# Performance work log

Hardware: AMD Instinct MI355X
Metric: run time of the kernel (lower is better)

The kernel has to match this reference:

```python
import jax, jax.numpy as jnp
import numpy as np

N_NODES = 50000
N_EDGES = 800000
IN_CH = 128
HID = 64
MLP_HID = 128
EPS = 1e-5


def setup_inputs() -> dict:
    key = jax.random.key(0)
    ks = iter(jax.random.split(key, 32))
    d = {}
    d['x'] = jax.random.normal(next(ks), (N_NODES, IN_CH), dtype=jnp.float32)
    d['edge_index'] = jax.random.randint(next(ks), (2, N_EDGES), 0, N_NODES, dtype=jnp.int64)

    def lin(k, out_c, in_c, scale=None):
        s = scale if scale is not None else 1.0 / np.sqrt(in_c)
        return jax.random.uniform(k, (out_c, in_c), jnp.float32, -s, s)

    # layer 0: in->hid, with residual linear
    d['Wl0'] = lin(next(ks), HID, IN_CH); d['bl0'] = jnp.zeros((HID,), jnp.float32)
    d['Wr0'] = lin(next(ks), HID, IN_CH)
    d['g0'] = jnp.ones((HID,), jnp.float32); d['be0'] = jnp.zeros((HID,), jnp.float32)
    d['rW0'] = lin(next(ks), HID, IN_CH); d['rb0'] = jnp.zeros((HID,), jnp.float32)
    # layers 1,2: hid->hid, identity residual
    for i in (1, 2):
        d[f'Wl{i}'] = lin(next(ks), HID, HID); d[f'bl{i}'] = jnp.zeros((HID,), jnp.float32)
        d[f'Wr{i}'] = lin(next(ks), HID, HID)
        d[f'g{i}'] = jnp.ones((HID,), jnp.float32); d[f'be{i}'] = jnp.zeros((HID,), jnp.float32)
    # edge MLP: 2*HID -> MLP_HID -> MLP_HID -> 1
    d['W1'] = lin(next(ks), MLP_HID, 2 * HID); d['b1'] = jnp.zeros((MLP_HID,), jnp.float32)
    d['W2'] = lin(next(ks), MLP_HID, MLP_HID); d['b2'] = jnp.zeros((MLP_HID,), jnp.float32)
    d['W3'] = lin(next(ks), 1, MLP_HID); d['b3'] = jnp.zeros((1,), jnp.float32)
    return d


def _res_sage_layer(x, src, tgt, Wl, bl, Wr, g, be, rW=None, rb=None):
    # SAGEConv (mean aggr): out = lin_l(mean_{j in N(i)} x_j) + lin_r(x_i)
    msg = x[src]                                              # [E, C] gather
    agg = jax.ops.segment_sum(msg, tgt, num_segments=N_NODES)
    cnt = jax.ops.segment_sum(jnp.ones((msg.shape[0],), x.dtype), tgt, num_segments=N_NODES)
    mean = agg / jnp.maximum(cnt, 1.0)[:, None]
    out = mean @ Wl.T + bl + x @ Wr.T
    # BatchNorm (training-mode batch statistics, biased var)
    mu = out.mean(axis=0)
    var = out.var(axis=0)
    out = (out - mu) * jax.lax.rsqrt(var + EPS) * g + be
    out = jax.nn.relu(out)
    res = x @ rW.T + rb if rW is not None else x
    return out + res


def reference(x, edge_index, Wl0, bl0, Wr0, g0, be0, rW0, rb0,
              Wl1, bl1, Wr1, g1, be1, Wl2, bl2, Wr2, g2, be2,
              W1, b1, W2, b2, W3, b3):
    src, tgt = edge_index[0], edge_index[1]
    h = _res_sage_layer(x, src, tgt, Wl0, bl0, Wr0, g0, be0, rW0, rb0)
    h = _res_sage_layer(h, src, tgt, Wl1, bl1, Wr1, g1, be1)
    h = _res_sage_layer(h, src, tgt, Wl2, bl2, Wr2, g2, be2)
    edge_repr = jnp.concatenate([h[src], h[tgt]], axis=1)     # [E, 2*HID]
    z = jax.nn.relu(edge_repr @ W1.T + b1)                    # dropout: eval mode (identity)
    z = jax.nn.relu(z @ W2.T + b2)
    return z @ W3.T + b3                                      # [E, 1]
```

## Files before the change

kernel.cpp:

```cpp
#include <hip/hip_runtime.h>
#include <hip/hip_bf16.h>

#define NN 50000
#define NE 800000
#define HID 64
#define EPSV 1e-5f
#define NBLK 196

typedef __attribute__((ext_vector_type(8))) short bf16x8;
typedef __attribute__((ext_vector_type(4))) float f32x4;
typedef __attribute__((ext_vector_type(4))) int int4v;

__device__ __forceinline__ ushort f2b(float f) {
    union { __hip_bfloat16 b; ushort u; } c;
    c.b = __float2bfloat16(f);
    return c.u;
}
__device__ __forceinline__ float b2f(ushort u) {
    return __uint_as_float(((unsigned int)u) << 16);
}

__global__ void prep_w_kernel(const float* __restrict__ W1, const float* __restrict__ W2,
                              ushort* __restrict__ W1b, ushort* __restrict__ W2b) {
    int i = blockIdx.x * 256 + threadIdx.x;
    if (i < 16384) W1b[i] = f2b(W1[i]);
    else           W2b[i - 16384] = f2b(W2[i - 16384]);
}

__global__ void prep_nodew_kernel(
    const float* __restrict__ Wl0, const float* __restrict__ Wr0, const float* __restrict__ rW0,
    const float* __restrict__ Wl1, const float* __restrict__ Wr1,
    const float* __restrict__ Wl2, const float* __restrict__ Wr2,
    ushort* __restrict__ wnb)
{
    int i = blockIdx.x * 256 + threadIdx.x;
    if      (i < 8192)  wnb[i] = f2b(Wl0[i]);
    else if (i < 16384) wnb[i] = f2b(Wr0[i - 8192]);
    else if (i < 24576) wnb[i] = f2b(rW0[i - 16384]);
    else if (i < 28672) wnb[i] = f2b(Wl1[i - 24576]);
    else if (i < 32768) wnb[i] = f2b(Wr1[i - 28672]);
    else if (i < 36864) wnb[i] = f2b(Wl2[i - 32768]);
    else if (i < 40960) wnb[i] = f2b(Wr2[i - 36864]);
}

__global__ void xcvt_kernel(const float* __restrict__ x, ushort* __restrict__ xq) {
    int i = blockIdx.x * 256 + threadIdx.x;
    float4 a = *(const float4*)&x[i * 8];
    float4 b = *(const float4*)&x[i * 8 + 4];
    union { ushort u[8]; int4v v; } pk;
    pk.u[0] = f2b(a.x); pk.u[1] = f2b(a.y); pk.u[2] = f2b(a.z); pk.u[3] = f2b(a.w);
    pk.u[4] = f2b(b.x); pk.u[5] = f2b(b.y); pk.u[6] = f2b(b.z); pk.u[7] = f2b(b.w);
    *(int4v*)&xq[i * 8] = pk.v;
}

__global__ void count_kernel(const int* __restrict__ tgt, int* __restrict__ icnt) {
    int e = blockIdx.x * 256 + threadIdx.x;
    if (e < NE) atomicAdd(&icnt[tgt[e]], 1);
}

__global__ void scan1_kernel(const int* __restrict__ icnt, int* __restrict__ off,
                             int* __restrict__ bsum) {
    __shared__ int s[256];
    const int t = threadIdx.x;
    const int i = blockIdx.x * 256 + t;
    int v = (i < NN) ? icnt[i] : 0;
    s[t] = v;
    __syncthreads();
    for (int d = 1; d < 256; d <<= 1) {
        int x = (t >= d) ? s[t - d] : 0;
        __syncthreads();
        s[t] += x;
        __syncthreads();
    }
    if (i < NN) off[i] = s[t];
    if (t == 255) bsum[blockIdx.x] = s[255];
}

__global__ void scan2_kernel(const int* __restrict__ bsum, int* __restrict__ bpre) {
    __shared__ int s[256];
    const int t = threadIdx.x;
    int v = (t < NBLK) ? bsum[t] : 0;
    s[t] = v;
    __syncthreads();
    for (int d = 1; d < 256; d <<= 1) {
        int x = (t >= d) ? s[t - d] : 0;
        __syncthreads();
        s[t] += x;
        __syncthreads();
    }
    if (t < NBLK) bpre[t] = s[t] - v;
}

__global__ void scan3_kernel(const int* __restrict__ icnt, const int* __restrict__ bpre,
                             int* __restrict__ off, int* __restrict__ woff) {
    const int i = blockIdx.x * 256 + threadIdx.x;
    if (i < NN) {
        int e = off[i] - icnt[i] + bpre[blockIdx.x];
        off[i] = e;
        woff[i] = e;
        if (i == NN - 1) off[NN] = NE;
    }
}

__global__ void fill_kernel(const int* __restrict__ src, const int* __restrict__ tgt,
                            int* __restrict__ woff, int* __restrict__ ebuf) {
    int e = blockIdx.x * 256 + threadIdx.x;
    if (e < NE) {
        int p = atomicAdd(&woff[tgt[e]], 1);
        ebuf[p] = src[e];
    }
}

template<int K>
__global__ __launch_bounds__(256) void proj_mfma_kernel(
    const ushort* __restrict__ Ab,
    const ushort* __restrict__ w0, const ushort* __restrict__ w1,
    const ushort* __restrict__ w2,
    const float* __restrict__ bias1, const float* __restrict__ bias2,
    ushort* __restrict__ xb, float* __restrict__ pre, float* __restrict__ res)
{
    __shared__ float sC[128][65];
    const int tid = threadIdx.x;
    const int wv = tid >> 6, lane = tid & 63;
    const int l15 = lane & 15, l4 = lane >> 4;
    const int seg = blockIdx.y;
    const ushort* W = (seg == 0) ? w0 : ((seg == 1) ? w1 : w2);
    const int n0 = blockIdx.x * 128;
    constexpr int KS = K / 32;

    bf16x8 wf[4][KS];
    #pragma unroll
    for (int n = 0; n < 4; n++)
        #pragma unroll
        for (int ks = 0; ks < KS; ks++)
            wf[n][ks] = *(const bf16x8*)&W[(n * 16 + l15) * K + ks * 32 + l4 * 8];

    f32x4 acc[2][4];
    #pragma unroll
    for (int m = 0; m < 2; m++)
        #pragma unroll
        for (int n = 0; n < 4; n++)
            acc[m][n] = (f32x4){0.f, 0.f, 0.f, 0.f};

    #pragma unroll
    for (int m = 0; m < 2; m++) {
        int row = n0 + wv * 32 + m * 16 + l15;
        if (row > NN - 1) row = NN - 1;
        #pragma unroll
        for (int ks = 0; ks < KS; ks++) {
            bf16x8 a = *(const bf16x8*)&Ab[(long)row * K + ks * 32 + l4 * 8];
            #pragma unroll
            for (int n = 0; n < 4; n++)
                acc[m][n] = __builtin_amdgcn_mfma_f32_16x16x32_bf16(a, wf[n][ks], acc[m][n], 0, 0, 0);
        }
    }
    #pragma unroll
    for (int m = 0; m < 2; m++)
        #pragma unroll
        for (int n = 0; n < 4; n++)
            #pragma unroll
            for (int r = 0; r < 4; r++)
                sC[wv * 32 + m * 16 + l4 * 4 + r][n * 16 + l15] = acc[m][n][r];
    __syncthreads();

    const int r = tid >> 1, ch = (tid & 1) * 32;
    const int node = n0 + r;
    if (node < NN) {
        if (seg == 0) {
            #pragma unroll
            for (int g = 0; g < 4; g++) {
                union { ushort u[8]; int4v v; } pk;
                #pragma unroll
                for (int j = 0; j < 8; j++)
                    pk.u[j] = f2b(sC[r][ch + g * 8 + j]);
                *(int4v*)&xb[(long)node * 64 + ch + g * 8] = pk.v;
            }
        } else {
            float* O = (seg == 1) ? pre : res;
            const float* bp = (seg == 1) ? bias1 : bias2;
            #pragma unroll
            for (int g = 0; g < 8; g++) {
                int c = ch + g * 4;
                float4 v = make_float4(sC[r][c + 0] + bp[c + 0], sC[r][c + 1] + bp[c + 1],
                                       sC[r][c + 2] + bp[c + 2], sC[r][c + 3] + bp[c + 3]);
                *(float4*)&O[(long)node * 64 + c] = v;
            }
        }
    }
}

__global__ __launch_bounds__(256) void gather_bn_kernel(
    const int* __restrict__ off, const int* __restrict__ ebuf,
    const ushort* __restrict__ xb,
    float* __restrict__ vbase,
    float* __restrict__ bnsum, float* __restrict__ bnsq)
{
    __shared__ float r1[4][64], r2[4][64];
    const int lane = threadIdx.x & 63;
    const int wid = __builtin_amdgcn_readfirstlane(threadIdx.x >> 6);
    float s = 0.f, q = 0.f;
    for (int n = blockIdx.x * 4 + wid; n < NN; n += gridDim.x * 4) {
        const int a = off[n], b = off[n + 1];
        float a0 = 0.f, a1 = 0.f, a2 = 0.f, a3 = 0.f;
        int p = a;
        for (; p + 4 <= b; p += 4) {
            int s0 = ebuf[p], s1 = ebuf[p + 1], s2 = ebuf[p + 2], s3 = ebuf[p + 3];
            a0 += b2f(xb[(long)s0 * 64 + lane]);
            a1 += b2f(xb[(long)s1 * 64 + lane]);
            a2 += b2f(xb[(long)s2 * 64 + lane]);
            a3 += b2f(xb[(long)s3 * 64 + lane]);
        }
        for (; p < b; ++p) a0 += b2f(xb[(long)ebuf[p] * 64 + lane]);
        float acc = (a0 + a1) + (a2 + a3);
        float v = acc / fmaxf((float)(b - a), 1.f) + vbase[(long)n * 64 + lane];
        vbase[(long)n * 64 + lane] = v;
        s += v; q += v * v;
    }
    r1[wid][lane] = s; r2[wid][lane] = q;
    __syncthreads();
    if (threadIdx.x < 64) {
        s = r1[0][lane] + r1[1][lane] + r1[2][lane] + r1[3][lane];
        q = r2[0][lane] + r2[1][lane] + r2[2][lane] + r2[3][lane];
        atomicAdd(&bnsum[lane], s);
        atomicAdd(&bnsq[lane], q);
    }
}

__global__ void apply_bn_kernel(const float* __restrict__ vbase,
                                const float* __restrict__ resbase,
                                const float* __restrict__ bnsum, const float* __restrict__ bnsq,
                                const float* __restrict__ g, const float* __restrict__ be,
                                float* __restrict__ h, ushort* __restrict__ hb)
{
    const float inv_n = 1.0f / (float)NN;
    const int stride = gridDim.x * 256;
    for (int i = blockIdx.x * 256 + threadIdx.x; i < NN * 16; i += stride) {
        int n = i >> 4;
        int c0 = (i & 15) * 4;
        float sc[4], sh[4];
        #pragma unroll
        for (int j = 0; j < 4; j++) {
            int c = c0 + j;
            float mu = bnsum[c] * inv_n;
            float var = bnsq[c] * inv_n - mu * mu;
            float rstd = rsqrtf(var + EPSV);
            sc[j] = g[c] * rstd;
            sh[j] = be[c] - mu * sc[j];
        }
        float4 v = *(const float4*)&vbase[(long)n * 64 + c0];
        float4 r = *(const float4*)&resbase[(long)n * 64 + c0];
        float4 o;
        o.x = fmaxf(fmaf(v.x, sc[0], sh[0]), 0.f) + r.x;
        o.y = fmaxf(fmaf(v.y, sc[1], sh[1]), 0.f) + r.y;
        o.z = fmaxf(fmaf(v.z, sc[2], sh[2]), 0.f) + r.z;
        o.w = fmaxf(fmaf(v.w, sc[3], sh[3]), 0.f) + r.w;
        *(float4*)&h[(long)n * 64 + c0] = o;
        union { ushort u[4]; uint2 v2; } p;
        p.u[0] = f2b(o.x); p.u[1] = f2b(o.y); p.u[2] = f2b(o.z); p.u[3] = f2b(o.w);
        *(uint2*)&hb[(long)n * 64 + c0] = p.v2;
    }
}

#define NTILE 6250
#define EMG 256
#define Z1B(row, usc) ((((row) * 272) + ((usc) * 2)) ^ ((((row) >> 1) & 7) << 4))

#define GATHER(tt)                                                        \
    do {                                                                  \
        int e0g = (t0 + (tt)) * 128;                                      \
        _Pragma("unroll")                                                 \
        for (int m = 0; m < 2; m++) {                                     \
            int e = e0g + we * 32 + m * 16 + l15;                         \
            const ushort* hs = hb + (long)src[e] * 64;                    \
            const ushort* ht = hb + (long)tgt[e] * 64;                    \
            ga[m][0] = *(const bf16x8*)&hs[l4 * 8];                       \
            ga[m][1] = *(const bf16x8*)&hs[32 + l4 * 8];                  \
            ga[m][2] = *(const bf16x8*)&ht[l4 * 8];                       \
            ga[m][3] = *(const bf16x8*)&ht[32 + l4 * 8];                  \
        }                                                                 \
    } while (0)

__global__ __launch_bounds__(512, 2) void edge_mlp_lds_kernel(
    const ushort* __restrict__ hb,
    const int* __restrict__ src, const int* __restrict__ tgt,
    const ushort* __restrict__ W1b, const ushort* __restrict__ W2b,
    const float* __restrict__ b1, const float* __restrict__ b2,
    const float* __restrict__ W3, const float* __restrict__ b3,
    float* __restrict__ out)
{
    __shared__ ushort wlds[32768];
    __shared__ ushort z1[128 * 136];
    __shared__ float red[2][2][128];

    const int tid = threadIdx.x;
    const int wid = tid >> 6, lane = tid & 63;
    const int l15 = lane & 15, l4 = lane >> 4;
    const int we = wid >> 1, wo = wid & 1;
    const int ocb = wo * 64;

    for (int c = tid; c < 4096; c += 512) {
        int layer = c >> 11, oc = (c >> 4) & 127, kc = c & 15;
        const ushort* Wsrc = layer ? W2b : W1b;
        int4v v = *(const int4v*)&Wsrc[oc * 128 + kc * 8];
        int byte = layer * 32768 + oc * 256 + ((kc * 16) ^ ((oc & 7) << 4));
        *(int4v*)((char*)wlds + byte) = v;
    }

    float b1v[4], b2v[4], w3v[4];
    #pragma unroll
    for (int n = 0; n < 4; n++) {
        int oc = ocb + n * 16 + l15;
        b1v[n] = b1[oc]; b2v[n] = b2[oc]; w3v[n] = W3[oc];
    }
    const float b3v = b3[0];

    const int bid = blockIdx.x;
    const int q = NTILE / EMG, r = NTILE % EMG;
    const int t0 = bid * q + (bid < r ? bid : r);
    const int nt = q + (bid < r ? 1 : 0);

    bf16x8 ga[2][4];
    GATHER(0);
    __syncthreads();

    for (int t = 0; t < nt; t++) {
        f32x4 acc[2][4];
        #pragma unroll
        for (int m = 0; m < 2; m++)
            #pragma unroll
            for (int n = 0; n < 4; n++)
                acc[m][n] = (f32x4){b1v[n], b1v[n], b1v[n], b1v[n]};
        #pragma unroll
        for (int ks = 0; ks < 4; ks++) {
            bf16x8 wf[4];
            #pragma unroll
            for (int n = 0; n < 4; n++) {
                int oc = ocb + n * 16 + l15;
                int byte = oc * 256 + (((ks * 4 + l4) * 16) ^ ((oc & 7) << 4));
                wf[n] = *(const bf16x8*)((const char*)wlds + byte);
            }
            #pragma unroll
            for (int m = 0; m < 2; m++)
                #pragma unroll
                for (int n = 0; n < 4; n++)
                    acc[m][n] = __builtin_amdgcn_mfma_f32_16x16x32_bf16(ga[m][ks], wf[n], acc[m][n], 0, 0, 0);
        }
        #pragma unroll
        for (int m = 0; m < 2; m++)
            #pragma unroll
            for (int n = 0; n < 4; n++) {
                int col = ocb + n * 16 + l15;
                #pragma unroll
                for (int rr = 0; rr < 4; rr++) {
                    int row = we * 32 + m * 16 + l4 * 4 + rr;
                    *(ushort*)((char*)z1 + Z1B(row, col)) = f2b(fmaxf(acc[m][n][rr], 0.f));
                }
            }
        __syncthreads();

        if (t + 1 < nt) GATHER(t + 1);

        f32x4 acc2[2][4];
        #pragma unroll
        for (int m = 0; m < 2; m++)
            #pragma unroll
            for (int n = 0; n < 4; n++)
                acc2[m][n] = (f32x4){b2v[n], b2v[n], b2v[n], b2v[n]};
        #pragma unroll
        for (int ks = 0; ks < 4; ks++) {
            bf16x8 wf[4];
            #pragma unroll
            for (int n = 0; n < 4; n++) {
                int oc = ocb + n * 16 + l15;
                int byte = 32768 + oc * 256 + (((ks * 4 + l4) * 16) ^ ((oc & 7) << 4));
                wf[n] = *(const bf16x8*)((const char*)wlds + byte);
            }
            bf16x8 a2[2];
            #pragma unroll
            for (int m = 0; m < 2; m++) {
                int erow = we * 32 + m * 16 + l15;
                a2[m] = *(const bf16x8*)((const char*)z1 + Z1B(erow, ks * 32 + l4 * 8));
            }
            #pragma unroll
            for (int m = 0; m < 2; m++)
                #pragma unroll
                for (int n = 0; n < 4; n++)
                    acc2[m][n] = __builtin_amdgcn_mfma_f32_16x16x32_bf16(a2[m], wf[n], acc2[m][n], 0, 0, 0);
        }

        #pragma unroll
        for (int m = 0; m < 2; m++)
            #pragma unroll
            for (int rr = 0; rr < 4; rr++) {
                float s = 0.f;
                #pragma unroll
                for (int n = 0; n < 4; n++)
                    s = fmaf(fmaxf(acc2[m][n][rr], 0.f), w3v[n], s);
                s += __shfl_xor(s, 1);
                s += __shfl_xor(s, 2);
                s += __shfl_xor(s, 4);
                s += __shfl_xor(s, 8);
                if (l15 == 0)
                    red[t & 1][wo][we * 32 + m * 16 + l4 * 4 + rr] = s;
            }
        __syncthreads();
        if (tid < 128)
            out[(t0 + t) * 128 + tid] = red[t & 1][0][tid] + red[t & 1][1][tid] + b3v;
    }
}

extern "C" void kernel_launch(void* const* d_in, const int* in_sizes, int n_in,
                              void* d_out, int out_size, void* d_ws, size_t ws_size,
                              hipStream_t stream)
{
    const float* x   = (const float*)d_in[0];
    const int*   ei  = (const int*)d_in[1];
    const int* src = ei;
    const int* tgt = ei + NE;
    const float* Wl0 = (const float*)d_in[2];
    const float* bl0 = (const float*)d_in[3];
    const float* Wr0 = (const float*)d_in[4];
    const float* g0  = (const float*)d_in[5];
    const float* be0 = (const float*)d_in[6];
    const float* rW0 = (const float*)d_in[7];
    const float* rb0 = (const float*)d_in[8];
    const float* Wl1 = (const float*)d_in[9];
    const float* bl1 = (const float*)d_in[10];
    const float* Wr1 = (const float*)d_in[11];
    const float* g1  = (const float*)d_in[12];
    const float* be1 = (const float*)d_in[13];
    const float* Wl2 = (const float*)d_in[14];
    const float* bl2 = (const float*)d_in[15];
    const float* Wr2 = (const float*)d_in[16];
    const float* g2  = (const float*)d_in[17];
    const float* be2 = (const float*)d_in[18];
    const float* W1  = (const float*)d_in[19];
    const float* b1  = (const float*)d_in[20];
    const float* W2  = (const float*)d_in[21];
    const float* b2  = (const float*)d_in[22];
    const float* W3  = (const float*)d_in[23];
    const float* b3  = (const float*)d_in[24];
    float* out = (float*)d_out;

    float* ws = (float*)d_ws;
    float*  pre  = ws;
    float*  res  = ws + 3200000;
    float*  hbuf = ws + 6400000;
    float*  bn   = ws + 9600000;
    float*  bnsum = bn, *bnsq = bn + 64;
    ushort* xb   = (ushort*)(ws + 9600256);
    ushort* hb   = (ushort*)(ws + 11200256);
    ushort* W1b  = (ushort*)(ws + 12800256);
    ushort* W2b  = W1b + 16384;
    int*    icnt = (int*)(ws + 12816640);
    int*    off  = icnt + 50000;
    int*    woff = off + 50001;
    int*    ebuf = woff + 50000;
    int*    bsum = ebuf + 800000;
    int*    bpre = bsum + 256;
    ushort* wnb  = (ushort*)(ws + 13767153);
    ushort* Wl0b = wnb;
    ushort* Wr0b = wnb + 8192;
    ushort* rW0b = wnb + 16384;
    ushort* Wl1b = wnb + 24576;
    ushort* Wr1b = wnb + 28672;
    ushort* Wl2b = wnb + 32768;
    ushort* Wr2b = wnb + 36864;
    ushort* xb16 = (ushort*)hbuf;

    prep_w_kernel<<<128, 256, 0, stream>>>(W1, W2, W1b, W2b);
    prep_nodew_kernel<<<160, 256, 0, stream>>>(Wl0, Wr0, rW0, Wl1, Wr1, Wl2, Wr2, wnb);
    xcvt_kernel<<<3125, 256, 0, stream>>>(x, xb16);
    hipMemsetAsync(icnt, 0, NN * sizeof(int), stream);
    count_kernel<<<NE / 256, 256, 0, stream>>>(tgt, icnt);
    scan1_kernel<<<NBLK, 256, 0, stream>>>(icnt, off, bsum);
    scan2_kernel<<<1, 256, 0, stream>>>(bsum, bpre);
    scan3_kernel<<<NBLK, 256, 0, stream>>>(icnt, bpre, off, woff);
    fill_kernel<<<NE / 256, 256, 0, stream>>>(src, tgt, woff, ebuf);

    dim3 g0g(391, 3), g12g(391, 2);

    hipMemsetAsync(bnsum, 0, 128 * sizeof(float), stream);
    proj_mfma_kernel<128><<<g0g, 256, 0, stream>>>(xb16, Wl0b, Wr0b, rW0b,
                                                   bl0, rb0, xb, pre, res);
    gather_bn_kernel<<<1024, 256, 0, stream>>>(off, ebuf, xb, pre, bnsum, bnsq);
    apply_bn_kernel<<<1024, 256, 0, stream>>>(pre, res, bnsum, bnsq, g0, be0, hbuf, hb);

    hipMemsetAsync(bnsum, 0, 128 * sizeof(float), stream);
    proj_mfma_kernel<64><<<g12g, 256, 0, stream>>>(hb, Wl1b, Wr1b, nullptr,
                                                   bl1, nullptr, xb, pre, res);
    gather_bn_kernel<<<1024, 256, 0, stream>>>(off, ebuf, xb, pre, bnsum, bnsq);
    apply_bn_kernel<<<1024, 256, 0, stream>>>(pre, hbuf, bnsum, bnsq, g1, be1, hbuf, hb);

    hipMemsetAsync(bnsum, 0, 128 * sizeof(float), stream);
    proj_mfma_kernel<64><<<g12g, 256, 0, stream>>>(hb, Wl2b, Wr2b, nullptr,
                                                   bl2, nullptr, xb, pre, res);
    gather_bn_kernel<<<1024, 256, 0, stream>>>(off, ebuf, xb, pre, bnsum, bnsq);
    apply_bn_kernel<<<1024, 256, 0, stream>>>(pre, hbuf, bnsum, bnsq, g2, be2, hbuf, hb);

    edge_mlp_lds_kernel<<<EMG, 512, 0, stream>>>(hb, src, tgt, W1b, W2b, b1, b2, W3, b3, out);
}
```

Measured before the change: 482.1 us.

## Make each wave own a full 32-edge strip in edge MLP, removing block barriers

Restructures the edge MLP kernel so each wave processes independent 32-edge strips across all 128 output channels, with a private LDS scratch for the layer-1 activations. This removes the per-tile __syncthreads barriers and the cross-wave reduction buffer, and each wave writes its outputs directly as float4. The cost is double the accumulator registers per wave (acc arrays of 2x8) and dropping the min-2-blocks launch bound, which may lower occupancy or cause spills. The z1 swizzle is replaced by a padded stride, so LDS bank conflicts may change.

```diff
diff --git a/kernel.cpp b/kernel.cpp
--- a/kernel.cpp
+++ b/kernel.cpp
@@ -261,16 +261,16 @@
     }
 }
 
-#define NTILE 6250
+#define NSTRIP 25000
 #define EMG 256
-#define Z1B(row, usc) ((((row) * 272) + ((usc) * 2)) ^ ((((row) >> 1) & 7) << 4))
-
-#define GATHER(tt)                                                        \
+#define ZSTR 136
+
+#define GATHER(ss)                                                        \
     do {                                                                  \
-        int e0g = (t0 + (tt)) * 128;                                      \
+        int e0g = (ss) * 32;                                              \
         _Pragma("unroll")                                                 \
         for (int m = 0; m < 2; m++) {                                     \
-            int e = e0g + we * 32 + m * 16 + l15;                         \
+            int e = e0g + m * 16 + l15;                                   \
             const ushort* hs = hb + (long)src[e] * 64;                    \
             const ushort* ht = hb + (long)tgt[e] * 64;                    \
             ga[m][0] = *(const bf16x8*)&hs[l4 * 8];                       \
@@ -280,7 +280,7 @@
         }                                                                 \
     } while (0)
 
-__global__ __launch_bounds__(512, 2) void edge_mlp_lds_kernel(
+__global__ __launch_bounds__(512) void edge_mlp_wave_kernel(
     const ushort* __restrict__ hb,
     const int* __restrict__ src, const int* __restrict__ tgt,
     const ushort* __restrict__ W1b, const ushort* __restrict__ W2b,
@@ -289,14 +289,11 @@
     float* __restrict__ out)
 {
     __shared__ ushort wlds[32768];
-    __shared__ ushort z1[128 * 136];
-    __shared__ float red[2][2][128];
+    __shared__ ushort z1[8][32 * ZSTR];
 
     const int tid = threadIdx.x;
     const int wid = tid >> 6, lane = tid & 63;
     const int l15 = lane & 15, l4 = lane >> 4;
-    const int we = wid >> 1, wo = wid & 1;
-    const int ocb = wo * 64;
 
     for (int c = tid; c < 4096; c += 512) {
         int layer = c >> 11, oc = (c >> 4) & 127, kc = c & 15;
@@ -306,106 +303,105 @@
         *(int4v*)((char*)wlds + byte) = v;
     }
 
-    float b1v[4], b2v[4], w3v[4];
+    float b1v[8], b2v[8], w3v[8];
     #pragma unroll
-    for (int n = 0; n < 4; n++) {
-        int oc = ocb + n * 16 + l15;
+    for (int n = 0; n < 8; n++) {
+        int oc = n * 16 + l15;
         b1v[n] = b1[oc]; b2v[n] = b2[oc]; w3v[n] = W3[oc];
     }
     const float b3v = b3[0];
 
     const int bid = blockIdx.x;
-    const int q = NTILE / EMG, r = NTILE % EMG;
+    const int q = NSTRIP / EMG, r = NSTRIP % EMG;
     const int t0 = bid * q + (bid < r ? bid : r);
     const int nt = q + (bid < r ? 1 : 0);
+    ushort* zw = z1[wid];
 
     bf16x8 ga[2][4];
-    GATHER(0);
+    if (wid < nt) GATHER(t0 + wid);
     __syncthreads();
 
-    for (int t = 0; t < nt; t++) {
-        f32x4 acc[2][4];
+    for (int j = wid; j < nt; j += 8) {
+        const int e0 = (t0 + j) * 32;
+
+        f32x4 acc[2][8];
         #pragma unroll
         for (int m = 0; m < 2; m++)
             #pragma unroll
-            for (int n = 0; n < 4; n++)
+            for (int n = 0; n < 8; n++)
                 acc[m][n] = (f32x4){b1v[n], b1v[n], b1v[n], b1v[n]};
         #pragma unroll
         for (int ks = 0; ks < 4; ks++) {
-            bf16x8 wf[4];
-            #pragma unroll
-            for (int n = 0; n < 4; n++) {
-                int oc = ocb + n * 16 + l15;
+            bf16x8 wf[8];
+            #pragma unroll
+            for (int n = 0; n < 8; n++) {
+                int oc = n * 16 + l15;
                 int byte = oc * 256 + (((ks * 4 + l4) * 16) ^ ((oc & 7) << 4));
                 wf[n] = *(const bf16x8*)((const char*)wlds + byte);
             }
             #pragma unroll
             for (int m = 0; m < 2; m++)
                 #pragma unroll
-                for (int n = 0; n < 4; n++)
+                for (int n = 0; n < 8; n++)
                     acc[m][n] = __builtin_amdgcn_mfma_f32_16x16x32_bf16(ga[m][ks], wf[n], acc[m][n], 0, 0, 0);
         }
         #pragma unroll
         for (int m = 0; m < 2; m++)
             #pragma unroll
-            for (int n = 0; n < 4; n++) {
-                int col = ocb + n * 16 + l15;
+            for (int n = 0; n < 8; n++) {
+                int col = n * 16 + l15;
                 #pragma unroll
-                for (int rr = 0; rr < 4; rr++) {
-                    int row = we * 32 + m * 16 + l4 * 4 + rr;
-                    *(ushort*)((char*)z1 + Z1B(row, col)) = f2b(fmaxf(acc[m][n][rr], 0.f));
-                }
-            }
-        __syncthreads();
-
-        if (t + 1 < nt) GATHER(t + 1);
-
-        f32x4 acc2[2][4];
+                for (int rr = 0; rr < 4; rr++)
+                    zw[(m * 16 + l4 * 4 + rr) * ZSTR + col] = f2b(fmaxf(acc[m][n][rr], 0.f));
+            }
+
+        if (j + 8 < nt) GATHER(t0 + j + 8);
+
+        f32x4 acc2[2][8];
         #pragma unroll
         for (int m = 0; m < 2; m++)
             #pragma unroll
-            for (int n = 0; n < 4; n++)
+            for (int n = 0; n < 8; n++)
                 acc2[m][n] = (f32x4){b2v[n], b2v[n], b2v[n], b2v[n]};
         #pragma unroll
         for (int ks = 0; ks < 4; ks++) {
-            bf16x8 wf[4];
-            #pragma unroll
-            for (int n = 0; n < 4; n++) {
-                int oc = ocb + n * 16 + l15;
+            bf16x8 wf[8];
+            #pragma unroll
+            for (int n = 0; n < 8; n++) {
+                int oc = n * 16 + l15;
                 int byte = 32768 + oc * 256 + (((ks * 4 + l4) * 16) ^ ((oc & 7) << 4));
                 wf[n] = *(const bf16x8*)((const char*)wlds + byte);
             }
             bf16x8 a2[2];
             #pragma unroll
-            for (int m = 0; m < 2; m++) {
-                int erow = we * 32 + m * 16 + l15;
-                a2[m] = *(const bf16x8*)((const char*)z1 + Z1B(erow, ks * 32 + l4 * 8));
-            }
+            for (int m = 0; m < 2; m++)
+                a2[m] = *(const bf16x8*)&zw[(m * 16 + l15) * ZSTR + ks * 32 + l4 * 8];
             #pragma unroll
             for (int m = 0; m < 2; m++)
                 #pragma unroll
-                for (int n = 0; n < 4; n++)
+                for (int n = 0; n < 8; n++)
                     acc2[m][n] = __builtin_amdgcn_mfma_f32_16x16x32_bf16(a2[m], wf[n], acc2[m][n], 0, 0, 0);
         }
 
         #pragma unroll
-        for (int m = 0; m < 2; m++)
+        for (int m = 0; m < 2; m++) {
+            float sv[4];
             #pragma unroll
             for (int rr = 0; rr < 4; rr++) {
                 float s = 0.f;
                 #pragma unroll
-                for (int n = 0; n < 4; n++)
+                for (int n = 0; n < 8; n++)
                     s = fmaf(fmaxf(acc2[m][n][rr], 0.f), w3v[n], s);
                 s += __shfl_xor(s, 1);
                 s += __shfl_xor(s, 2);
                 s += __shfl_xor(s, 4);
                 s += __shfl_xor(s, 8);
-                if (l15 == 0)
-                    red[t & 1][wo][we * 32 + m * 16 + l4 * 4 + rr] = s;
-            }
-        __syncthreads();
-        if (tid < 128)
-            out[(t0 + t) * 128 + tid] = red[t & 1][0][tid] + red[t & 1][1][tid] + b3v;
+                sv[rr] = s + b3v;
+            }
+            if (l15 == 0)
+                *(float4*)&out[e0 + m * 16 + l4 * 4] =
+                    make_float4(sv[0], sv[1], sv[2], sv[3]);
+        }
     }
 }
 
@@ -498,5 +494,5 @@
     gather_bn_kernel<<<1024, 256, 0, stream>>>(off, ebuf, xb, pre, bnsum, bnsq);
     apply_bn_kernel<<<1024, 256, 0, stream>>>(pre, hbuf, bnsum, bnsq, g2, be2, hbuf, hb);
 
-    edge_mlp_lds_kernel<<<EMG, 512, 0, stream>>>(hb, src, tgt, W1b, W2b, b1, b2, W3, b3, out);
-}
+    edge_mlp_wave_kernel<<<EMG, 512, 0, stream>>>(hb, src, tgt, W1b, W2b, b1, b2, W3, b3, out);
+}
```

After: 430.4 us. 10.7% less time.
